# Optimization experiments

Hardware: AMD Instinct MI355X
Metric: run time of the kernel (lower is better)

Reference implementation:

```python
import jax, jax.numpy as jnp
import numpy as np

G, NPG = 100, 500
N = G * NPG            # 50000 nodes, contiguous equal-size graphs
IN, H = 128, 256
L = 3                  # num_layers
K = 3                  # knn k (loop=True -> self included)
E = 16 * N             # 800000 edges

def setup_inputs():
    key = jax.random.key(0)
    k = jax.random.split(key, 8)
    x = jax.random.normal(k[0], (N, IN), jnp.float32)
    batch = jnp.repeat(jnp.arange(G, dtype=jnp.int32), NPG)
    gid = jax.random.randint(k[1], (E,), 0, G)
    src = jax.random.randint(k[2], (E,), 0, NPG) + gid * NPG
    dst = jax.random.randint(k[3], (E,), 0, NPG) + gid * NPG
    edge_index = jnp.stack([src, dst]).astype(jnp.int32)
    def lin(kk, fin, fout):
        return (jax.random.normal(kk, (fin, fout), jnp.float32) / np.sqrt(fin)).astype(jnp.float32)
    inp = dict(x=x, edge_index=edge_index, batch=batch)
    inp["emb_W"] = lin(k[4], IN, H); inp["emb_b"] = jnp.zeros((H,), jnp.float32)
    inp["conv_W"] = jnp.stack([lin(jax.random.fold_in(k[5], i), H, H) for i in range(L)])
    inp["conv_b"] = jnp.zeros((L, H), jnp.float32)
    inp["fconv_W"] = jnp.stack([lin(jax.random.fold_in(k[6], i), H, H) for i in range(L)])
    inp["fconv_b"] = jnp.zeros((L, H), jnp.float32)
    inp["norm_w"] = jnp.ones((L, H), jnp.float32); inp["norm_b"] = jnp.zeros((L, H), jnp.float32); inp["norm_ms"] = jnp.ones((L, H), jnp.float32)
    inp["fnorm_w"] = jnp.ones((L, H), jnp.float32); inp["fnorm_b"] = jnp.zeros((L, H), jnp.float32); inp["fnorm_ms"] = jnp.ones((L, H), jnp.float32)
    inp["gate_W"] = lin(k[7], 2 * H, H); inp["gate_b"] = jnp.zeros((H,), jnp.float32)
    return inp

def _gcn_conv(h, src, dst, W, b):
    # GCNConv: add self loops, symmetric deg^-1/2 normalization
    m = h @ W                                     # [N,H]
    loop = jnp.arange(N, dtype=src.dtype)
    s2 = jnp.concatenate([src, loop]); d2 = jnp.concatenate([dst, loop])
    deg = jax.ops.segment_sum(jnp.ones_like(d2, jnp.float32), d2, num_segments=N)
    dinv = jnp.where(deg > 0, jax.lax.rsqrt(deg), 0.0)
    coef = (dinv[s2] * dinv[d2])[:, None]
    return jax.ops.segment_sum(m[s2] * coef, d2, num_segments=N) + b

def _graph_norm(x, batch, w, b, ms, cnt):
    # PyG GraphNorm: out = w * (x - ms*mean) / sqrt(var + eps) + b, per-graph stats
    mean = jax.ops.segment_sum(x, batch, num_segments=G) / cnt
    out = x - mean[batch] * ms
    var = jax.ops.segment_sum(out * out, batch, num_segments=G) / cnt
    return w * out * jax.lax.rsqrt(var + 1e-5)[batch] + b

def _knn_graph(x):
    # per-graph cosine knn, loop=True (self has sim 1 and is kept)
    xr = x.reshape(G, NPG, -1)
    xn = xr / (jnp.linalg.norm(xr, axis=-1, keepdims=True) + 1e-12)
    sim = jnp.einsum('gnh,gmh->gnm', xn, xn)      # [G,NPG,NPG]
    _, idx = jax.lax.top_k(sim, K)                # [G,NPG,K]
    offs = (jnp.arange(G) * NPG)[:, None, None]
    src = (idx + offs).reshape(-1)
    dst = jnp.broadcast_to(jnp.arange(N).reshape(G, NPG, 1), (G, NPG, K)).reshape(-1)
    return src.astype(jnp.int32), dst.astype(jnp.int32)

def reference(x, edge_index, batch, emb_W, emb_b, conv_W, conv_b, norm_w, norm_b, norm_ms, fconv_W, fconv_b, fnorm_w, fnorm_b, fnorm_ms, gate_W, gate_b):
    cnt = jax.ops.segment_sum(jnp.ones((N,), jnp.float32), batch, num_segments=G)[:, None]
    h = x @ emb_W + emb_b
    fsrc, fdst = _knn_graph(h)
    src, dst = edge_index[0], edge_index[1]
    all_x = []
    for i in range(L - 1):   # eval mode: dropout is identity
        prev = h
        h = _gcn_conv(h, src, dst, conv_W[i], conv_b[i])
        h = jax.nn.leaky_relu(_graph_norm(h, batch, norm_w[i], norm_b[i], norm_ms[i], cnt))
        f = _gcn_conv(h, fsrc, fdst, fconv_W[i], fconv_b[i])
        f = jax.nn.leaky_relu(_graph_norm(f, batch, fnorm_w[i], fnorm_b[i], fnorm_ms[i], cnt))
        gate = jax.nn.sigmoid(jnp.concatenate([h, f], axis=-1) @ gate_W + gate_b)
        h = gate * h + (1.0 - gate) * f + prev
        all_x.append(h)
    # faithful to source: for i in range(L): += pool(all_x[i-1])  (Python negative indexing!)
    gf = jnp.zeros((G, H), jnp.float32)
    for i in range(L):
        gf = gf + jax.ops.segment_sum(all_x[i - 1], batch, num_segments=G) / cnt
    return gf
```

## Files before the change

kernel.cpp:

```cpp
#include <hip/hip_runtime.h>
#include <math.h>

#define NN 50000
#define GG 100
#define NPGc 500
#define HH 256
#define IND 128

typedef __attribute__((ext_vector_type(8))) short short8v;
typedef __attribute__((ext_vector_type(4))) float f32x4;

__device__ __forceinline__ ushort f2bf(float f) {
    union { float f; unsigned u; } v; v.f = f;
    unsigned r = (v.u + 0x7fffu + ((v.u >> 16) & 1u)) >> 16;
    return (ushort)r;
}
__device__ __forceinline__ float bf2f(ushort h) {
    union { unsigned u; float f; } v; v.u = ((unsigned)h) << 16;
    return v.f;
}

__global__ void wcvt(const float* __restrict__ src, ushort* __restrict__ dst, int K, int N)
{
    int i = blockIdx.x * 256 + threadIdx.x;
    if (i < K * N) {
        int n = i / K, k = i % K;
        dst[i] = f2bf(src[(size_t)k * N + n]);
    }
}

__global__ __launch_bounds__(256)
void gemm_mfma(const float* __restrict__ A, const float* __restrict__ A2,
               const ushort* __restrict__ Wt, const float* __restrict__ bias,
               float* __restrict__ C, int M, int K, int lda, int mode,
               const float* __restrict__ hn, const float* __restrict__ fn,
               const float* __restrict__ prev)
{
    __shared__ ushort As[128][64];
    __shared__ ushort Bs[128][64];
    const int tid = threadIdx.x;
    const int lane = tid & 63;
    const int w = tid >> 6;
    const int wr = (w >> 1) * 64, wc = (w & 1) * 64;
    const int row0 = blockIdx.x * 128, col0 = blockIdx.y * 128;
    const int lr = lane & 15, lk = (lane >> 4) * 8;
    f32x4 acc[4][4] = {};

    for (int k0 = 0; k0 < K; k0 += 64) {
        __syncthreads();
        #pragma unroll
        for (int it = 0; it < 4; ++it) {
            int c = it * 256 + tid;
            int row = c >> 3, col = (c & 7) * 8;
            int gr = row0 + row; if (gr > M - 1) gr = M - 1;
            const float* Ap = A; int kk = k0 + col;
            if (A2 != nullptr && kk >= 256) { Ap = A2; kk -= 256; }
            const float* s = &Ap[(size_t)gr * lda + kk];
            float4 v0 = *(const float4*)s;
            float4 v1 = *(const float4*)(s + 4);
            union { ushort u[8]; int4 q; } pk;
            pk.u[0] = f2bf(v0.x); pk.u[1] = f2bf(v0.y); pk.u[2] = f2bf(v0.z); pk.u[3] = f2bf(v0.w);
            pk.u[4] = f2bf(v1.x); pk.u[5] = f2bf(v1.y); pk.u[6] = f2bf(v1.z); pk.u[7] = f2bf(v1.w);
            *(int4*)&As[row][col] = pk.q;
        }
        #pragma unroll
        for (int it = 0; it < 4; ++it) {
            int c = it * 256 + tid;
            int n = c >> 3, k = (c & 7) * 8;
            *(int4*)&Bs[n][k] = *(const int4*)&Wt[(size_t)(col0 + n) * K + k0 + k];
        }
        __syncthreads();
        #pragma unroll
        for (int ks = 0; ks < 2; ++ks) {
            short8v av[4], bv[4];
            #pragma unroll
            for (int m = 0; m < 4; ++m) av[m] = *(const short8v*)&As[wr + m * 16 + lr][ks * 32 + lk];
            #pragma unroll
            for (int n = 0; n < 4; ++n) bv[n] = *(const short8v*)&Bs[wc + n * 16 + lr][ks * 32 + lk];
            #pragma unroll
            for (int m = 0; m < 4; ++m)
                #pragma unroll
                for (int n = 0; n < 4; ++n)
                    acc[m][n] = __builtin_amdgcn_mfma_f32_16x16x32_bf16(av[m], bv[n], acc[m][n], 0, 0, 0);
        }
    }
    const int fr = (lane >> 4) * 4;
    if (mode == 0) {
        #pragma unroll
        for (int n = 0; n < 4; ++n) {
            int col = col0 + wc + n * 16 + lr;
            float bb = bias ? bias[col] : 0.f;
            #pragma unroll
            for (int m = 0; m < 4; ++m) {
                int rbase = row0 + wr + m * 16 + fr;
                #pragma unroll
                for (int r = 0; r < 4; ++r) {
                    int row = rbase + r;
                    if (row < M) C[(size_t)row * HH + col] = acc[m][n][r] + bb;
                }
            }
        }
    } else {
        #pragma unroll
        for (int n = 0; n < 4; ++n) {
            int col = col0 + wc + n * 16 + lr;
            float gb = bias[col];
            #pragma unroll
            for (int m = 0; m < 4; ++m) {
                int rbase = row0 + wr + m * 16 + fr;
                #pragma unroll
                for (int r = 0; r < 4; ++r) {
                    int row = rbase + r;
                    if (row < M) {
                        size_t o = (size_t)row * HH + col;
                        float z = acc[m][n][r] + gb;
                        float s = 1.f / (1.f + expf(-z));
                        C[o] = s * hn[o] + (1.f - s) * fn[o] + prev[o];
                    }
                }
            }
        }
    }
}

__global__ __launch_bounds__(256)
void sim_mfma(const float* __restrict__ xn, float* __restrict__ sim)
{
    __shared__ ushort Ah[128][64], Al[128][64], Bh[128][64], Bl[128][64];
    const int g = blockIdx.z;
    const float* X = xn + (size_t)g * NPGc * HH;
    float* S = sim + (size_t)g * NPGc * NPGc;
    const int tid = threadIdx.x;
    const int lane = tid & 63;
    const int w = tid >> 6;
    const int wr = (w >> 1) * 64, wc = (w & 1) * 64;
    const int row0 = blockIdx.x * 128, col0 = blockIdx.y * 128;
    const int lr = lane & 15, lk = (lane >> 4) * 8;
    f32x4 acc[4][4] = {};

    for (int k0 = 0; k0 < HH; k0 += 64) {
        __syncthreads();
        #pragma unroll
        for (int it = 0; it < 4; ++it) {
            int c = it * 256 + tid;
            int row = c >> 3, col = (c & 7) * 8;
            int gr = row0 + row; if (gr > NPGc - 1) gr = NPGc - 1;
            const float* s = &X[(size_t)gr * HH + k0 + col];
            float4 v0 = *(const float4*)s;
            float4 v1 = *(const float4*)(s + 4);
            float vv[8] = { v0.x, v0.y, v0.z, v0.w, v1.x, v1.y, v1.z, v1.w };
            union { ushort u[8]; int4 q; } ph, pl;
            #pragma unroll
            for (int j = 0; j < 8; ++j) {
                ushort h = f2bf(vv[j]);
                ph.u[j] = h;
                pl.u[j] = f2bf(vv[j] - bf2f(h));
            }
            *(int4*)&Ah[row][col] = ph.q;
            *(int4*)&Al[row][col] = pl.q;
        }
        #pragma unroll
        for (int it = 0; it < 4; ++it) {
            int c = it * 256 + tid;
            int row = c >> 3, col = (c & 7) * 8;
            int gr = col0 + row; if (gr > NPGc - 1) gr = NPGc - 1;
            const float* s = &X[(size_t)gr * HH + k0 + col];
            float4 v0 = *(const float4*)s;
            float4 v1 = *(const float4*)(s + 4);
            float vv[8] = { v0.x, v0.y, v0.z, v0.w, v1.x, v1.y, v1.z, v1.w };
            union { ushort u[8]; int4 q; } ph, pl;
            #pragma unroll
            for (int j = 0; j < 8; ++j) {
                ushort h = f2bf(vv[j]);
                ph.u[j] = h;
                pl.u[j] = f2bf(vv[j] - bf2f(h));
            }
            *(int4*)&Bh[row][col] = ph.q;
            *(int4*)&Bl[row][col] = pl.q;
        }
        __syncthreads();
        #pragma unroll
        for (int ks = 0; ks < 2; ++ks) {
            short8v ah[4], al[4], bh[4], bl[4];
            #pragma unroll
            for (int m = 0; m < 4; ++m) {
                ah[m] = *(const short8v*)&Ah[wr + m * 16 + lr][ks * 32 + lk];
                al[m] = *(const short8v*)&Al[wr + m * 16 + lr][ks * 32 + lk];
            }
            #pragma unroll
            for (int n = 0; n < 4; ++n) {
                bh[n] = *(const short8v*)&Bh[wc + n * 16 + lr][ks * 32 + lk];
                bl[n] = *(const short8v*)&Bl[wc + n * 16 + lr][ks * 32 + lk];
            }
            #pragma unroll
            for (int m = 0; m < 4; ++m)
                #pragma unroll
                for (int n = 0; n < 4; ++n) {
                    acc[m][n] = __builtin_amdgcn_mfma_f32_16x16x32_bf16(ah[m], bh[n], acc[m][n], 0, 0, 0);
                    acc[m][n] = __builtin_amdgcn_mfma_f32_16x16x32_bf16(ah[m], bl[n], acc[m][n], 0, 0, 0);
                    acc[m][n] = __builtin_amdgcn_mfma_f32_16x16x32_bf16(al[m], bh[n], acc[m][n], 0, 0, 0);
                }
        }
    }
    const int fr = (lane >> 4) * 4;
    #pragma unroll
    for (int n = 0; n < 4; ++n) {
        int col = col0 + wc + n * 16 + lr;
        if (col >= NPGc) continue;
        #pragma unroll
        for (int m = 0; m < 4; ++m) {
            int rbase = row0 + wr + m * 16 + fr;
            #pragma unroll
            for (int r = 0; r < 4; ++r) {
                int row = rbase + r;
                if (row < NPGc) S[(size_t)row * NPGc + col] = acc[m][n][r];
            }
        }
    }
}

__global__ __launch_bounds__(256)
void row_normalize(const float* __restrict__ h, float* __restrict__ xn)
{
    int n = blockIdx.x, c = threadIdx.x;
    float v = h[(size_t)n * HH + c];
    __shared__ float red[256];
    red[c] = v * v;
    __syncthreads();
    for (int s = 128; s > 0; s >>= 1) {
        if (c < s) red[c] += red[c + s];
        __syncthreads();
    }
    float norm = sqrtf(red[0]);
    xn[(size_t)n * HH + c] = v / (norm + 1e-12f);
}

__device__ __forceinline__ bool tk_better(float va, int ia, float vb, int ib)
{
    return (va > vb) || (va == vb && ia < ib);
}

__global__ __launch_bounds__(256)
void topk_kernel(const float* __restrict__ sim, int* __restrict__ fsrc)
{
    int row = blockIdx.x * 4 + (threadIdx.x >> 6);
    if (row >= NN) return;
    int lane = threadIdx.x & 63;
    int g = row / NPGc, i = row % NPGc;
    const float* srow = sim + (size_t)g * NPGc * NPGc + (size_t)i * NPGc;
    float v0 = -2.f, v1 = -2.f, v2 = -2.f;
    int i0 = 0x7fffffff, i1 = 0x7fffffff, i2 = 0x7fffffff;
    for (int j = lane; j < NPGc; j += 64) {
        float v = srow[j];
        if (tk_better(v, j, v0, i0))      { v2 = v1; i2 = i1; v1 = v0; i1 = i0; v0 = v; i0 = j; }
        else if (tk_better(v, j, v1, i1)) { v2 = v1; i2 = i1; v1 = v;  i1 = j; }
        else if (tk_better(v, j, v2, i2)) { v2 = v;  i2 = j; }
    }
    for (int off = 32; off; off >>= 1) {
        float w0 = __shfl_xor(v0, off), w1 = __shfl_xor(v1, off), w2 = __shfl_xor(v2, off);
        int   j0 = __shfl_xor(i0, off), j1 = __shfl_xor(i1, off), j2 = __shfl_xor(i2, off);
        float avv[3] = { v0, v1, v2 }, bvv[3] = { w0, w1, w2 };
        int   aii[3] = { i0, i1, i2 }, bii[3] = { j0, j1, j2 };
        float rv[3]; int ri[3];
        int p = 0, q = 0;
        #pragma unroll
        for (int t = 0; t < 3; ++t) {
            bool takeA = tk_better(avv[p], aii[p], bvv[q], bii[q]);
            rv[t] = takeA ? avv[p] : bvv[q];
            ri[t] = takeA ? aii[p] : bii[q];
            if (takeA) ++p; else ++q;
        }
        v0 = rv[0]; v1 = rv[1]; v2 = rv[2];
        i0 = ri[0]; i1 = ri[1]; i2 = ri[2];
    }
    if (lane == 0) {
        int base = g * NPGc;
        fsrc[row * 3 + 0] = base + i0;
        fsrc[row * 3 + 1] = base + i1;
        fsrc[row * 3 + 2] = base + i2;
    }
}

__global__ void hist_kernel(const int* __restrict__ dst, int* __restrict__ cnt, int nE)
{
    int e = blockIdx.x * 256 + threadIdx.x;
    if (e < nE) atomicAdd(&cnt[dst[e]], 1);
}

__global__ void scan1_kernel(const int* __restrict__ in, int* __restrict__ out,
                             int* __restrict__ bsum, int n)
{
    __shared__ int sh[256];
    int t = threadIdx.x;
    int i = blockIdx.x * 256 + t;
    int v = (i < n) ? in[i] : 0;
    sh[t] = v;
    __syncthreads();
    for (int s = 1; s < 256; s <<= 1) {
        int tv = (t >= s) ? sh[t - s] : 0;
        __syncthreads();
        sh[t] += tv;
        __syncthreads();
    }
    if (i < n) out[i] = sh[t] - v;
    if (t == 255) bsum[blockIdx.x] = sh[255];
}

__global__ void scan2_kernel(int* __restrict__ bsum, int nb)
{
    __shared__ int sh[256];
    int t = threadIdx.x;
    int v = (t < nb) ? bsum[t] : 0;
    sh[t] = v;
    __syncthreads();
    for (int s = 1; s < 256; s <<= 1) {
        int tv = (t >= s) ? sh[t - s] : 0;
        __syncthreads();
        sh[t] += tv;
        __syncthreads();
    }
    if (t < nb) bsum[t] = sh[t] - v;
}

__global__ void scan3_kernel(int* __restrict__ out, const int* __restrict__ bsum, int n)
{
    int i = blockIdx.x * 256 + threadIdx.x;
    if (i < n) out[i] += bsum[blockIdx.x];
}

__global__ void fill_kernel(const int* __restrict__ src, const int* __restrict__ dst,
                            const int* __restrict__ row_ptr, int* __restrict__ cursor,
                            int* __restrict__ sorted_src, int nE)
{
    int e = blockIdx.x * 256 + threadIdx.x;
    if (e < nE) {
        int d = dst[e];
        int pos = row_ptr[d] + atomicAdd(&cursor[d], 1);
        sorted_src[pos] = src[e];
    }
}

__global__ void dinv_kernel(const int* __restrict__ cnt, float* __restrict__ dinv, int n)
{
    int i = blockIdx.x * 256 + threadIdx.x;
    if (i < n) dinv[i] = rsqrtf((float)cnt[i] + 1.0f);
}

__global__ __launch_bounds__(256)
void gcn_gather(const float* __restrict__ m, const int* __restrict__ row_ptr,
                const int* __restrict__ cnt, const int* __restrict__ srcs,
                const float* __restrict__ dinv, const float* __restrict__ bias,
                float* __restrict__ out)
{
    int n = blockIdx.x, c = threadIdx.x;
    float dn = dinv[n];
    float acc = m[(size_t)n * HH + c] * dn;
    int s0 = row_ptr[n], e0 = s0 + cnt[n];
    for (int e = s0; e < e0; ++e) {
        int s = srcs[e];
        acc += m[(size_t)s * HH + c] * dinv[s];
    }
    out[(size_t)n * HH + c] = acc * dn + bias[c];
}

__global__ __launch_bounds__(256)
void fgcn_gather(const float* __restrict__ m, const int* __restrict__ fsrc,
                 const float* __restrict__ bias, float* __restrict__ out)
{
    int n = blockIdx.x, c = threadIdx.x;
    int s0 = fsrc[n * 3], s1 = fsrc[n * 3 + 1], s2 = fsrc[n * 3 + 2];
    float acc = m[(size_t)n * HH + c] + m[(size_t)s0 * HH + c]
              + m[(size_t)s1 * HH + c] + m[(size_t)s2 * HH + c];
    out[(size_t)n * HH + c] = 0.25f * acc + bias[c];
}

__global__ __launch_bounds__(256)
void norm_stats(const float* __restrict__ x, float* __restrict__ S1, float* __restrict__ S2)
{
    int g = blockIdx.x, chunk = blockIdx.y, c = threadIdx.x;
    int r0 = chunk * 63, r1 = min(r0 + 63, NPGc);
    float s1 = 0.f, s2 = 0.f;
    for (int r = r0; r < r1; ++r) {
        float v = x[((size_t)(g * NPGc + r)) * HH + c];
        s1 += v; s2 += v * v;
    }
    atomicAdd(&S1[g * HH + c], s1);
    atomicAdd(&S2[g * HH + c], s2);
}

__global__ __launch_bounds__(256)
void norm_apply(float* __restrict__ x, const float* __restrict__ S1, const float* __restrict__ S2,
                const float* __restrict__ w, const float* __restrict__ b,
                const float* __restrict__ ms)
{
    int n = blockIdx.x, c = threadIdx.x;
    int g = n / NPGc;
    size_t o = (size_t)n * HH + c;
    float v = x[o];
    float mean = S1[g * HH + c] / (float)NPGc;
    float mm = mean * ms[c];
    float var = S2[g * HH + c] / (float)NPGc - 2.f * mm * mean + mm * mm;
    float outv = w[c] * (v - mm) * rsqrtf(var + 1e-5f) + b[c];
    x[o] = outv > 0.f ? outv : 0.01f * outv;
}

__global__ __launch_bounds__(256)
void pool_kernel(const float* __restrict__ X0, const float* __restrict__ X1,
                 float* __restrict__ out)
{
    int g = blockIdx.x, c = threadIdx.x;
    float s0 = 0.f, s1 = 0.f;
    for (int r = 0; r < NPGc; ++r) {
        size_t o = ((size_t)(g * NPGc + r)) * HH + c;
        s0 += X0[o];
        s1 += X1[o];
    }
    out[g * HH + c] = (s0 + 2.f * s1) / (float)NPGc;
}

__global__ void sentinel_kernel(float* out, int n)
{
    int i = blockIdx.x * 256 + threadIdx.x;
    if (i < n) out[i] = 12345.0f;
}

extern "C" void kernel_launch(void* const* d_in, const int* in_sizes, int n_in,
                              void* d_out, int out_size, void* d_ws, size_t ws_size,
                              hipStream_t stream)
{
    const float* x       = (const float*)d_in[0];
    const int* edge_idx  = (const int*)d_in[1];
    const float* emb_W   = (const float*)d_in[3];
    const float* emb_b   = (const float*)d_in[4];
    const float* conv_W  = (const float*)d_in[5];
    const float* conv_b  = (const float*)d_in[6];
    const float* fconv_W = (const float*)d_in[7];
    const float* fconv_b = (const float*)d_in[8];
    const float* norm_w  = (const float*)d_in[9];
    const float* norm_b  = (const float*)d_in[10];
    const float* norm_ms = (const float*)d_in[11];
    const float* fnorm_w = (const float*)d_in[12];
    const float* fnorm_b = (const float*)d_in[13];
    const float* fnorm_ms= (const float*)d_in[14];
    const float* gate_W  = (const float*)d_in[15];
    const float* gate_b  = (const float*)d_in[16];

    const int E = in_sizes[1] / 2;
    const int* esrc = edge_idx;
    const int* edst = edge_idx + E;

    const size_t NHf = (size_t)NN * HH;
    char* p = (char*)d_ws;
    auto alloc = [&](size_t bytes) { char* r = p; p += (bytes + 255) & ~(size_t)255; return r; };
    float* B0 = (float*)alloc(NHf * 4);
    float* B1 = (float*)alloc(NHf * 4);
    float* B2 = (float*)alloc(NHf * 4);
    float* B3 = (float*)alloc(NHf * 4);
    float* sim = B2;
    int* sorted_src = (int*)alloc((size_t)E * 4);
    int* row_ptr    = (int*)alloc((size_t)NN * 4);
    int* deg_cnt    = (int*)alloc((size_t)NN * 4);
    int* cursor     = (int*)alloc((size_t)NN * 4);
    float* dinv     = (float*)alloc((size_t)NN * 4);
    int* fsrc       = (int*)alloc((size_t)NN * 3 * 4);
    float* S1       = (float*)alloc((size_t)GG * HH * 4);
    float* S2       = (float*)alloc((size_t)GG * HH * 4);
    int* bsum       = (int*)alloc(1024);
    ushort* wts     = (ushort*)alloc((size_t)425984 * 2);
    size_t needed = (size_t)(p - (char*)d_ws);
    if (ws_size < needed) {
        sentinel_kernel<<<(out_size + 255) / 256, 256, 0, stream>>>((float*)d_out, out_size);
        return;
    }
    ushort* embWt  = wts;
    ushort* convWt0 = wts + 32768;
    ushort* convWt1 = wts + 32768 + 65536;
    ushort* fconvWt0 = wts + 163840;
    ushort* fconvWt1 = wts + 163840 + 65536;
    ushort* gateWt  = wts + 294912;

    const int nScanB = (NN + 255) / 256;

    hipMemsetAsync(deg_cnt, 0, (size_t)NN * 4, stream);
    hipMemsetAsync(cursor, 0, (size_t)NN * 4, stream);

    wcvt<<<(32768 + 255) / 256, 256, 0, stream>>>(emb_W, embWt, IND, HH);
    wcvt<<<(65536 + 255) / 256, 256, 0, stream>>>(conv_W, convWt0, HH, HH);
    wcvt<<<(65536 + 255) / 256, 256, 0, stream>>>(conv_W + 65536, convWt1, HH, HH);
    wcvt<<<(65536 + 255) / 256, 256, 0, stream>>>(fconv_W, fconvWt0, HH, HH);
    wcvt<<<(65536 + 255) / 256, 256, 0, stream>>>(fconv_W + 65536, fconvWt1, HH, HH);
    wcvt<<<(131072 + 255) / 256, 256, 0, stream>>>(gate_W, gateWt, 2 * HH, HH);

    dim3 ggrid((NN + 127) / 128, 2);
    gemm_mfma<<<ggrid, 256, 0, stream>>>(x, nullptr, embWt, emb_b, B0, NN, IND, IND, 0,
                                         nullptr, nullptr, nullptr);

    hist_kernel<<<(E + 255) / 256, 256, 0, stream>>>(edst, deg_cnt, E);
    scan1_kernel<<<nScanB, 256, 0, stream>>>(deg_cnt, row_ptr, bsum, NN);
    scan2_kernel<<<1, 256, 0, stream>>>(bsum, nScanB);
    scan3_kernel<<<nScanB, 256, 0, stream>>>(row_ptr, bsum, NN);
    fill_kernel<<<(E + 255) / 256, 256, 0, stream>>>(esrc, edst, row_ptr, cursor, sorted_src, E);
    dinv_kernel<<<(NN + 255) / 256, 256, 0, stream>>>(deg_cnt, dinv, NN);

    row_normalize<<<NN, 256, 0, stream>>>(B0, B1);
    dim3 sgrid(4, 4, GG);
    sim_mfma<<<sgrid, 256, 0, stream>>>(B1, sim);
    topk_kernel<<<(NN + 3) / 4, 256, 0, stream>>>(sim, fsrc);

    float* h  = B0;
    float* mb = B1;
    dim3 ngrid(GG, 8);
    for (int i = 0; i < 2; ++i) {
        const ushort* Wc = (i == 0) ? convWt0 : convWt1;
        const ushort* Wf = (i == 0) ? fconvWt0 : fconvWt1;
        const float* bc  = conv_b  + (size_t)i * HH;
        const float* bf  = fconv_b + (size_t)i * HH;
        gemm_mfma<<<ggrid, 256, 0, stream>>>(h, nullptr, Wc, nullptr, mb, NN, HH, HH, 0,
                                             nullptr, nullptr, nullptr);
        gcn_gather<<<NN, 256, 0, stream>>>(mb, row_ptr, deg_cnt, sorted_src, dinv, bc, B2);
        hipMemsetAsync(S1, 0, (size_t)2 * GG * HH * 4, stream);
        norm_stats<<<ngrid, 256, 0, stream>>>(B2, S1, S2);
        norm_apply<<<NN, 256, 0, stream>>>(B2, S1, S2, norm_w + i * HH, norm_b + i * HH,
                                           norm_ms + i * HH);
        gemm_mfma<<<ggrid, 256, 0, stream>>>(B2, nullptr, Wf, nullptr, mb, NN, HH, HH, 0,
                                             nullptr, nullptr, nullptr);
        fgcn_gather<<<NN, 256, 0, stream>>>(mb, fsrc, bf, B3);
        hipMemsetAsync(S1, 0, (size_t)2 * GG * HH * 4, stream);
        norm_stats<<<ngrid, 256, 0, stream>>>(B3, S1, S2);
        norm_apply<<<NN, 256, 0, stream>>>(B3, S1, S2, fnorm_w + i * HH, fnorm_b + i * HH,
                                           fnorm_ms + i * HH);
        gemm_mfma<<<ggrid, 256, 0, stream>>>(B2, B3, gateWt, gate_b, mb, NN, 2 * HH, HH, 1,
                                             B2, B3, h);
        float* t = h; h = mb; mb = t;
    }
    pool_kernel<<<GG, 256, 0, stream>>>(mb, h, (float*)d_out);
}
```

Measured before the change: 1.409 ms.

## Fuse similarity GEMM with top-3 selection and precompute bf16 hi/lo split

Merges the per-graph similarity MFMA and the top-k kernel into one kernel that stages 64x128 similarity tiles in shared memory and keeps a running top-3 per row. This removes the 100x500x500 float similarity matrix write and re-read. Row normalization now emits bf16 hi/lo halves directly, so the split is done once per element instead of in every tile load. The fused kernel reads operands straight from global memory without LDS staging, and it launches only 800 blocks, which may leave parallelism low and expose load latency.

```diff
diff --git a/kernel.cpp b/kernel.cpp
--- a/kernel.cpp
+++ b/kernel.cpp
@@ -124,103 +124,7 @@
 }
 
 __global__ __launch_bounds__(256)
-void sim_mfma(const float* __restrict__ xn, float* __restrict__ sim)
-{
-    __shared__ ushort Ah[128][64], Al[128][64], Bh[128][64], Bl[128][64];
-    const int g = blockIdx.z;
-    const float* X = xn + (size_t)g * NPGc * HH;
-    float* S = sim + (size_t)g * NPGc * NPGc;
-    const int tid = threadIdx.x;
-    const int lane = tid & 63;
-    const int w = tid >> 6;
-    const int wr = (w >> 1) * 64, wc = (w & 1) * 64;
-    const int row0 = blockIdx.x * 128, col0 = blockIdx.y * 128;
-    const int lr = lane & 15, lk = (lane >> 4) * 8;
-    f32x4 acc[4][4] = {};
-
-    for (int k0 = 0; k0 < HH; k0 += 64) {
-        __syncthreads();
-        #pragma unroll
-        for (int it = 0; it < 4; ++it) {
-            int c = it * 256 + tid;
-            int row = c >> 3, col = (c & 7) * 8;
-            int gr = row0 + row; if (gr > NPGc - 1) gr = NPGc - 1;
-            const float* s = &X[(size_t)gr * HH + k0 + col];
-            float4 v0 = *(const float4*)s;
-            float4 v1 = *(const float4*)(s + 4);
-            float vv[8] = { v0.x, v0.y, v0.z, v0.w, v1.x, v1.y, v1.z, v1.w };
-            union { ushort u[8]; int4 q; } ph, pl;
-            #pragma unroll
-            for (int j = 0; j < 8; ++j) {
-                ushort h = f2bf(vv[j]);
-                ph.u[j] = h;
-                pl.u[j] = f2bf(vv[j] - bf2f(h));
-            }
-            *(int4*)&Ah[row][col] = ph.q;
-            *(int4*)&Al[row][col] = pl.q;
-        }
-        #pragma unroll
-        for (int it = 0; it < 4; ++it) {
-            int c = it * 256 + tid;
-            int row = c >> 3, col = (c & 7) * 8;
-            int gr = col0 + row; if (gr > NPGc - 1) gr = NPGc - 1;
-            const float* s = &X[(size_t)gr * HH + k0 + col];
-            float4 v0 = *(const float4*)s;
-            float4 v1 = *(const float4*)(s + 4);
-            float vv[8] = { v0.x, v0.y, v0.z, v0.w, v1.x, v1.y, v1.z, v1.w };
-            union { ushort u[8]; int4 q; } ph, pl;
-            #pragma unroll
-            for (int j = 0; j < 8; ++j) {
-                ushort h = f2bf(vv[j]);
-                ph.u[j] = h;
-                pl.u[j] = f2bf(vv[j] - bf2f(h));
-            }
-            *(int4*)&Bh[row][col] = ph.q;
-            *(int4*)&Bl[row][col] = pl.q;
-        }
-        __syncthreads();
-        #pragma unroll
-        for (int ks = 0; ks < 2; ++ks) {
-            short8v ah[4], al[4], bh[4], bl[4];
-            #pragma unroll
-            for (int m = 0; m < 4; ++m) {
-                ah[m] = *(const short8v*)&Ah[wr + m * 16 + lr][ks * 32 + lk];
-                al[m] = *(const short8v*)&Al[wr + m * 16 + lr][ks * 32 + lk];
-            }
-            #pragma unroll
-            for (int n = 0; n < 4; ++n) {
-                bh[n] = *(const short8v*)&Bh[wc + n * 16 + lr][ks * 32 + lk];
-                bl[n] = *(const short8v*)&Bl[wc + n * 16 + lr][ks * 32 + lk];
-            }
-            #pragma unroll
-            for (int m = 0; m < 4; ++m)
-                #pragma unroll
-                for (int n = 0; n < 4; ++n) {
-                    acc[m][n] = __builtin_amdgcn_mfma_f32_16x16x32_bf16(ah[m], bh[n], acc[m][n], 0, 0, 0);
-                    acc[m][n] = __builtin_amdgcn_mfma_f32_16x16x32_bf16(ah[m], bl[n], acc[m][n], 0, 0, 0);
-                    acc[m][n] = __builtin_amdgcn_mfma_f32_16x16x32_bf16(al[m], bh[n], acc[m][n], 0, 0, 0);
-                }
-        }
-    }
-    const int fr = (lane >> 4) * 4;
-    #pragma unroll
-    for (int n = 0; n < 4; ++n) {
-        int col = col0 + wc + n * 16 + lr;
-        if (col >= NPGc) continue;
-        #pragma unroll
-        for (int m = 0; m < 4; ++m) {
-            int rbase = row0 + wr + m * 16 + fr;
-            #pragma unroll
-            for (int r = 0; r < 4; ++r) {
-                int row = rbase + r;
-                if (row < NPGc) S[(size_t)row * NPGc + col] = acc[m][n][r];
-            }
-        }
-    }
-}
-
-__global__ __launch_bounds__(256)
-void row_normalize(const float* __restrict__ h, float* __restrict__ xn)
+void row_norm_hl(const float* __restrict__ h, ushort* __restrict__ xh, ushort* __restrict__ xl)
 {
     int n = blockIdx.x, c = threadIdx.x;
     float v = h[(size_t)n * HH + c];
@@ -232,7 +136,10 @@
         __syncthreads();
     }
     float norm = sqrtf(red[0]);
-    xn[(size_t)n * HH + c] = v / (norm + 1e-12f);
+    float xn = v / (norm + 1e-12f);
+    ushort hi = f2bf(xn);
+    xh[(size_t)n * HH + c] = hi;
+    xl[(size_t)n * HH + c] = f2bf(xn - bf2f(hi));
 }
 
 __device__ __forceinline__ bool tk_better(float va, int ia, float vb, int ib)
@@ -240,44 +147,124 @@
     return (va > vb) || (va == vb && ia < ib);
 }
 
-__global__ __launch_bounds__(256)
-void topk_kernel(const float* __restrict__ sim, int* __restrict__ fsrc)
-{
-    int row = blockIdx.x * 4 + (threadIdx.x >> 6);
-    if (row >= NN) return;
-    int lane = threadIdx.x & 63;
-    int g = row / NPGc, i = row % NPGc;
-    const float* srow = sim + (size_t)g * NPGc * NPGc + (size_t)i * NPGc;
-    float v0 = -2.f, v1 = -2.f, v2 = -2.f;
-    int i0 = 0x7fffffff, i1 = 0x7fffffff, i2 = 0x7fffffff;
-    for (int j = lane; j < NPGc; j += 64) {
-        float v = srow[j];
-        if (tk_better(v, j, v0, i0))      { v2 = v1; i2 = i1; v1 = v0; i1 = i0; v0 = v; i0 = j; }
-        else if (tk_better(v, j, v1, i1)) { v2 = v1; i2 = i1; v1 = v;  i1 = j; }
-        else if (tk_better(v, j, v2, i2)) { v2 = v;  i2 = j; }
-    }
-    for (int off = 32; off; off >>= 1) {
-        float w0 = __shfl_xor(v0, off), w1 = __shfl_xor(v1, off), w2 = __shfl_xor(v2, off);
-        int   j0 = __shfl_xor(i0, off), j1 = __shfl_xor(i1, off), j2 = __shfl_xor(i2, off);
-        float avv[3] = { v0, v1, v2 }, bvv[3] = { w0, w1, w2 };
-        int   aii[3] = { i0, i1, i2 }, bii[3] = { j0, j1, j2 };
-        float rv[3]; int ri[3];
-        int p = 0, q = 0;
-        #pragma unroll
-        for (int t = 0; t < 3; ++t) {
-            bool takeA = tk_better(avv[p], aii[p], bvv[q], bii[q]);
-            rv[t] = takeA ? avv[p] : bvv[q];
-            ri[t] = takeA ? aii[p] : bii[q];
-            if (takeA) ++p; else ++q;
-        }
-        v0 = rv[0]; v1 = rv[1]; v2 = rv[2];
-        i0 = ri[0]; i1 = ri[1]; i2 = ri[2];
-    }
-    if (lane == 0) {
-        int base = g * NPGc;
-        fsrc[row * 3 + 0] = base + i0;
-        fsrc[row * 3 + 1] = base + i1;
-        fsrc[row * 3 + 2] = base + i2;
+__device__ __forceinline__ void ins3(float v, int i,
+                                     float& a0, int& b0, float& a1, int& b1,
+                                     float& a2, int& b2)
+{
+    if (tk_better(v, i, a0, b0))      { a2 = a1; b2 = b1; a1 = a0; b1 = b0; a0 = v; b0 = i; }
+    else if (tk_better(v, i, a1, b1)) { a2 = a1; b2 = b1; a1 = v;  b1 = i; }
+    else if (tk_better(v, i, a2, b2)) { a2 = v;  b2 = i; }
+}
+
+__global__ __launch_bounds__(256)
+void simtopk(const ushort* __restrict__ xnh, const ushort* __restrict__ xnl,
+             int* __restrict__ fsrc)
+{
+    __shared__ float St[64][129];
+    const int g = blockIdx.y;
+    const int row0 = blockIdx.x * 64;
+    const int tid = threadIdx.x;
+    const int lane = tid & 63;
+    const int w = tid >> 6;
+    const int lr = lane & 15, lkb = (lane >> 4) * 8;
+    const int fr = (lane >> 4) * 4;
+    const size_t base = (size_t)g * NPGc * HH;
+
+    const ushort* aph[4]; const ushort* apl[4];
+    #pragma unroll
+    for (int m = 0; m < 4; ++m) {
+        int r = row0 + m * 16 + lr; if (r > NPGc - 1) r = NPGc - 1;
+        aph[m] = xnh + base + (size_t)r * HH + lkb;
+        apl[m] = xnl + base + (size_t)r * HH + lkb;
+    }
+
+    float rv0 = -2.f, rv1 = -2.f, rv2 = -2.f;
+    int ri0 = 0x7fffffff, ri1 = 0x7fffffff, ri2 = 0x7fffffff;
+
+    for (int ct = 0; ct < 4; ++ct) {
+        const int col0 = ct * 128;
+        const ushort* bph[2]; const ushort* bpl[2];
+        #pragma unroll
+        for (int n = 0; n < 2; ++n) {
+            int cidx = col0 + w * 32 + n * 16 + lr; if (cidx > NPGc - 1) cidx = NPGc - 1;
+            bph[n] = xnh + base + (size_t)cidx * HH + lkb;
+            bpl[n] = xnl + base + (size_t)cidx * HH + lkb;
+        }
+        f32x4 acc[4][2] = {};
+        #pragma unroll
+        for (int k0 = 0; k0 < HH; k0 += 32) {
+            short8v ah[4], al[4], bh[2], bl[2];
+            #pragma unroll
+            for (int m = 0; m < 4; ++m) {
+                ah[m] = *(const short8v*)(aph[m] + k0);
+                al[m] = *(const short8v*)(apl[m] + k0);
+            }
+            #pragma unroll
+            for (int n = 0; n < 2; ++n) {
+                bh[n] = *(const short8v*)(bph[n] + k0);
+                bl[n] = *(const short8v*)(bpl[n] + k0);
+            }
+            #pragma unroll
+            for (int m = 0; m < 4; ++m)
+                #pragma unroll
+                for (int n = 0; n < 2; ++n) {
+                    acc[m][n] = __builtin_amdgcn_mfma_f32_16x16x32_bf16(ah[m], bh[n], acc[m][n], 0, 0, 0);
+                    acc[m][n] = __builtin_amdgcn_mfma_f32_16x16x32_bf16(ah[m], bl[n], acc[m][n], 0, 0, 0);
+                    acc[m][n] = __builtin_amdgcn_mfma_f32_16x16x32_bf16(al[m], bh[n], acc[m][n], 0, 0, 0);
+                }
+        }
+        #pragma unroll
+        for (int m = 0; m < 4; ++m)
+            #pragma unroll
+            for (int n = 0; n < 2; ++n)
+                #pragma unroll
+                for (int r = 0; r < 4; ++r)
+                    St[m * 16 + fr + r][w * 32 + n * 16 + lr] = acc[m][n][r];
+        __syncthreads();
+
+        int r16 = lane & 15, cg = lane >> 4;
+        int srow = w * 16 + r16;
+        float v0 = -2.f, v1 = -2.f, v2 = -2.f;
+        int i0 = 0x7fffffff, i1 = 0x7fffffff, i2 = 0x7fffffff;
+        int cmax = NPGc - col0; if (cmax > 128) cmax = 128;
+        for (int t = 0; t < 32; ++t) {
+            int c = cg + 4 * t;
+            if (c < cmax) {
+                float v = St[srow][c];
+                ins3(v, col0 + c, v0, i0, v1, i1, v2, i2);
+            }
+        }
+        for (int off = 16; off <= 32; off <<= 1) {
+            float w0 = __shfl_xor(v0, off), w1 = __shfl_xor(v1, off), w2 = __shfl_xor(v2, off);
+            int   j0 = __shfl_xor(i0, off), j1 = __shfl_xor(i1, off), j2 = __shfl_xor(i2, off);
+            float avv[3] = { v0, v1, v2 }, bvv[3] = { w0, w1, w2 };
+            int   aii[3] = { i0, i1, i2 }, bii[3] = { j0, j1, j2 };
+            float rv[3]; int ri[3];
+            int p = 0, q = 0;
+            #pragma unroll
+            for (int t = 0; t < 3; ++t) {
+                bool takeA = tk_better(avv[p], aii[p], bvv[q], bii[q]);
+                rv[t] = takeA ? avv[p] : bvv[q];
+                ri[t] = takeA ? aii[p] : bii[q];
+                if (takeA) ++p; else ++q;
+            }
+            v0 = rv[0]; v1 = rv[1]; v2 = rv[2];
+            i0 = ri[0]; i1 = ri[1]; i2 = ri[2];
+        }
+        ins3(v0, i0, rv0, ri0, rv1, ri1, rv2, ri2);
+        ins3(v1, i1, rv0, ri0, rv1, ri1, rv2, ri2);
+        ins3(v2, i2, rv0, ri0, rv1, ri1, rv2, ri2);
+        __syncthreads();
+    }
+
+    if ((lane >> 4) == 0) {
+        int rl = w * 16 + (lane & 15);
+        if (row0 + rl < NPGc) {
+            int rg = g * NPGc + row0 + rl;
+            fsrc[rg * 3 + 0] = g * NPGc + ri0;
+            fsrc[rg * 3 + 1] = g * NPGc + ri1;
+            fsrc[rg * 3 + 2] = g * NPGc + ri2;
+        }
     }
 }
 
@@ -456,7 +443,8 @@
     float* B1 = (float*)alloc(NHf * 4);
     float* B2 = (float*)alloc(NHf * 4);
     float* B3 = (float*)alloc(NHf * 4);
-    float* sim = B2;
+    ushort* xnh = (ushort*)B2;
+    ushort* xnl = xnh + NHf;
     int* sorted_src = (int*)alloc((size_t)E * 4);
     int* row_ptr    = (int*)alloc((size_t)NN * 4);
     int* deg_cnt    = (int*)alloc((size_t)NN * 4);
@@ -472,7 +460,7 @@
         sentinel_kernel<<<(out_size + 255) / 256, 256, 0, stream>>>((float*)d_out, out_size);
         return;
     }
-    ushort* embWt  = wts;
+    ushort* embWt   = wts;
     ushort* convWt0 = wts + 32768;
     ushort* convWt1 = wts + 32768 + 65536;
     ushort* fconvWt0 = wts + 163840;
@@ -502,10 +490,9 @@
     fill_kernel<<<(E + 255) / 256, 256, 0, stream>>>(esrc, edst, row_ptr, cursor, sorted_src, E);
     dinv_kernel<<<(NN + 255) / 256, 256, 0, stream>>>(deg_cnt, dinv, NN);
 
-    row_normalize<<<NN, 256, 0, stream>>>(B0, B1);
-    dim3 sgrid(4, 4, GG);
-    sim_mfma<<<sgrid, 256, 0, stream>>>(B1, sim);
-    topk_kernel<<<(NN + 3) / 4, 256, 0, stream>>>(sim, fsrc);
+    row_norm_hl<<<NN, 256, 0, stream>>>(B0, xnh, xnl);
+    dim3 sgrid(8, GG);
+    simtopk<<<sgrid, 256, 0, stream>>>(xnh, xnl, fsrc);
 
     float* h  = B0;
     float* mb = B1;
```

Result: slower. 1.584 ms (+12.4%).
